# Optimization experiments

Hardware: AMD Instinct MI355X
Metric: run time of the kernel (lower is better)

Reference implementation:

```python
import jax, jax.numpy as jnp
import numpy as np

N_NODES = 50000
N_EDGES = 1600000
IN_CH, HID, OUT = 116, 256, 2


def setup_inputs() -> dict:
    key = jax.random.key(0)
    ks = jax.random.split(key, 8)
    x = jax.random.normal(ks[0], (N_NODES, IN_CH), dtype=jnp.float32)
    edge_index = jax.random.randint(ks[1], (2, N_EDGES), 0, N_NODES, dtype=jnp.int64)
    # GCNConv weights: layer l maps d_in -> d_out via x @ W + b (W stored [d_in, d_out])
    def glorot(k, di, do):
        s = jnp.sqrt(6.0 / (di + do)).astype(jnp.float32)
        return jax.random.uniform(k, (di, do), jnp.float32, -s, s)
    W1 = glorot(ks[2], IN_CH, HID); b1 = jnp.zeros((HID,), jnp.float32)
    W2 = glorot(ks[3], HID, HID);   b2 = jnp.zeros((HID,), jnp.float32)
    W3 = glorot(ks[4], HID, OUT);   b3 = jnp.zeros((OUT,), jnp.float32)
    return {"x": x, "edge_index": edge_index,
            "W1": W1, "b1": b1, "W2": W2, "b2": b2, "W3": W3, "b3": b3}


def _gcn_conv(h, W, b, src, dst, dinv):
    # PyG GCNConv (normalize=True, add_self_loops=True):
    #   out = D^{-1/2} (A + I) D^{-1/2} (h W) + b, deg counts in-edges + self loop
    hw = h @ W  # [N, d_out]
    coeff = dinv[src] * dinv[dst]                      # [E]
    msg = hw[src] * coeff[:, None]                     # [E, d_out]
    agg = jax.ops.segment_sum(msg, dst, num_segments=h.shape[0])
    agg = agg + hw * (dinv * dinv)[:, None]            # self-loop term
    return agg + b


def reference(x, edge_index, W1, b1, W2, b2, W3, b3):
    src, dst = edge_index[0], edge_index[1]
    n = x.shape[0]
    deg = jax.ops.segment_sum(jnp.ones_like(dst, dtype=x.dtype), dst, num_segments=n) + 1.0
    dinv = jax.lax.rsqrt(deg)
    h = jax.nn.relu(_gcn_conv(x, W1, b1, src, dst, dinv))
    h = jax.nn.relu(_gcn_conv(h, W2, b2, src, dst, dinv))
    out = _gcn_conv(h, W3, b3, src, dst, dinv)  # last layer: no activation (eval mode, no dropout)
    return out
```

## Files before the change

kernel.cpp:

```cpp
#include <hip/hip_runtime.h>
#include <hip/hip_bf16.h>
#include <stdint.h>

#define NN 50000
#define NE 1600000
#define INC 116
#define XBP 128
#define K1P 128
#define HID 256
#define OUTC 2

typedef float f32x4 __attribute__((ext_vector_type(4)));
typedef short s16x8 __attribute__((ext_vector_type(8)));

__device__ __forceinline__ ushort f2bf(float v) {
    uint32_t u = __float_as_uint(v);
    return (ushort)((u + 0x7FFFu + ((u >> 16) & 1u)) >> 16);
}
__device__ __forceinline__ float bf2f(ushort b) {
    return __uint_as_float(((uint32_t)b) << 16);
}
__device__ __forceinline__ float bflo(uint32_t u) { return __uint_as_float(u << 16); }
__device__ __forceinline__ float bfhi(uint32_t u) { return __uint_as_float(u & 0xFFFF0000u); }

__global__ void detect_fmt(const int* __restrict__ ebuf, int* __restrict__ flag) {
    int v = ebuf[2 * threadIdx.x + 1];
    unsigned long long b = __ballot(v != 0);
    if (threadIdx.x == 0) flag[0] = (b == 0ULL) ? 1 : 0;
}

__device__ __forceinline__ int edge_at(const int* __restrict__ ebuf, int is64, int idx) {
    return is64 ? ebuf[2 * idx] : ebuf[idx];
}

__global__ void deg_hist(const int* __restrict__ ebuf, const int* __restrict__ flag,
                         int* __restrict__ cnt) {
    int e = blockIdx.x * blockDim.x + threadIdx.x;
    if (e >= NE) return;
    int is64 = flag[0];
    int d = edge_at(ebuf, is64, NE + e);
    atomicAdd(&cnt[d], 1);
}

__global__ void dinv_kernel(const int* __restrict__ cnt, float* __restrict__ dinv) {
    int n = blockIdx.x * blockDim.x + threadIdx.x;
    if (n < NN) dinv[n] = rsqrtf((float)cnt[n] + 1.0f);
}

__global__ void scan1(const int* __restrict__ cnt, int* __restrict__ rowptr,
                      int* __restrict__ bsum) {
    __shared__ int s[256];
    int tid = threadIdx.x;
    int i = blockIdx.x * 256 + tid;
    int v = (i < NN) ? cnt[i] : 0;
    s[tid] = v;
    __syncthreads();
    for (int off = 1; off < 256; off <<= 1) {
        int t = (tid >= off) ? s[tid - off] : 0;
        __syncthreads();
        s[tid] += t;
        __syncthreads();
    }
    if (i < NN) rowptr[i] = s[tid] - v;
    if (tid == 255) bsum[blockIdx.x] = s[255];
}

__global__ void scan2(int* __restrict__ bsum, int nblocks) {
    __shared__ int s[256];
    int tid = threadIdx.x;
    int v = (tid < nblocks) ? bsum[tid] : 0;
    s[tid] = v;
    __syncthreads();
    for (int off = 1; off < 256; off <<= 1) {
        int t = (tid >= off) ? s[tid - off] : 0;
        __syncthreads();
        s[tid] += t;
        __syncthreads();
    }
    if (tid < nblocks) bsum[tid] = s[tid] - v;
}

__global__ void scan3(int* __restrict__ rowptr, const int* __restrict__ bsum,
                      int* __restrict__ fillpos) {
    int i = blockIdx.x * 256 + threadIdx.x;
    if (i < NN) {
        int r = rowptr[i] + bsum[blockIdx.x];
        rowptr[i] = r;
        fillpos[i] = r;
        if (i == NN - 1) rowptr[NN] = NE;
    }
}

__global__ void __launch_bounds__(256)
fill_csr2(const int* __restrict__ ebuf, const int* __restrict__ flag,
          int* __restrict__ fillpos, int* __restrict__ col) {
    int rng = blockIdx.x & 7;
    int lo = rng * (NN / 8), hi = lo + (NN / 8);
    int is64 = flag[0];
    int stride = (gridDim.x >> 3) * 256;
    for (int e = (blockIdx.x >> 3) * 256 + threadIdx.x; e < NE; e += stride) {
        int d = edge_at(ebuf, is64, NE + e);
        if (d >= lo && d < hi) {
            int s = edge_at(ebuf, is64, e);
            int p = atomicAdd(&fillpos[d], 1);
            col[p] = s;
        }
    }
}

__global__ void conv_x(const float* __restrict__ x, ushort* __restrict__ xb) {
    int i = blockIdx.x * 256 + threadIdx.x;
    if (i >= NN * XBP) return;
    int n = i >> 7, c = i & 127;
    xb[i] = (c < INC) ? f2bf(x[(size_t)n * INC + c]) : (ushort)0;
}

__global__ void decomp_w1(const float* __restrict__ W, ushort* __restrict__ hi,
                          ushort* __restrict__ lo) {
    int i = blockIdx.x * 256 + threadIdx.x;
    int n = i >> 7, k = i & 127;
    float v = (k < INC) ? W[k * HID + n] : 0.f;
    ushort h = f2bf(v);
    hi[n * K1P + k] = h;
    lo[n * K1P + k] = f2bf(v - bf2f(h));
}

__global__ void decomp_w2(const float* __restrict__ W, ushort* __restrict__ hi,
                          ushort* __restrict__ lo) {
    int i = blockIdx.x * 256 + threadIdx.x;
    int n = i >> 8, k = i & 255;
    float v = W[k * HID + n];
    ushort h = f2bf(v);
    hi[n * HID + k] = h;
    lo[n * HID + k] = f2bf(v - bf2f(h));
}

__global__ void __launch_bounds__(256)
agg1b(const ushort* __restrict__ xb, const float* __restrict__ x,
      const float* __restrict__ dinv, const int* __restrict__ rowptr,
      const int* __restrict__ col, ushort* __restrict__ ohi, ushort* __restrict__ olo) {
    __shared__ float red[16][16][8];
    int n = blockIdx.x, tid = threadIdx.x;
    int g = tid >> 4, c = tid & 15;
    int beg = rowptr[n], end = rowptr[n + 1];
    {
        float a0=0.f,a1=0.f,a2=0.f,a3=0.f,a4=0.f,a5=0.f,a6=0.f,a7=0.f;
        const ushort* hc = xb + c * 8;
        int j = beg + g;
        for (; j + 16 < end; j += 32) {
            int s0 = col[j], s1 = col[j + 16];
            float w0 = dinv[s0], w1 = dinv[s1];
            uint4 u0 = *(const uint4*)(hc + (size_t)s0 * XBP);
            uint4 u1 = *(const uint4*)(hc + (size_t)s1 * XBP);
            a0 += w0 * bflo(u0.x) + w1 * bflo(u1.x);
            a1 += w0 * bfhi(u0.x) + w1 * bfhi(u1.x);
            a2 += w0 * bflo(u0.y) + w1 * bflo(u1.y);
            a3 += w0 * bfhi(u0.y) + w1 * bfhi(u1.y);
            a4 += w0 * bflo(u0.z) + w1 * bflo(u1.z);
            a5 += w0 * bfhi(u0.z) + w1 * bfhi(u1.z);
            a6 += w0 * bflo(u0.w) + w1 * bflo(u1.w);
            a7 += w0 * bfhi(u0.w) + w1 * bfhi(u1.w);
        }
        if (j < end) {
            int s0 = col[j];
            float w0 = dinv[s0];
            uint4 u0 = *(const uint4*)(hc + (size_t)s0 * XBP);
            a0 += w0 * bflo(u0.x); a1 += w0 * bfhi(u0.x);
            a2 += w0 * bflo(u0.y); a3 += w0 * bfhi(u0.y);
            a4 += w0 * bflo(u0.z); a5 += w0 * bfhi(u0.z);
            a6 += w0 * bflo(u0.w); a7 += w0 * bfhi(u0.w);
        }
        red[g][c][0]=a0; red[g][c][1]=a1; red[g][c][2]=a2; red[g][c][3]=a3;
        red[g][c][4]=a4; red[g][c][5]=a5; red[g][c][6]=a6; red[g][c][7]=a7;
    }
    __syncthreads();
    int t = tid;
    if (t < K1P) {
        float s = 0.f;
        #pragma unroll
        for (int gg = 0; gg < 16; ++gg) s += red[gg][t >> 3][t & 7];
        float self = (t < INC) ? x[(size_t)n * INC + t] : 0.f;
        float dn = dinv[n];
        float r = dn * (s + dn * self);
        ushort h = f2bf(r);
        ohi[(size_t)n * K1P + t] = h;
        olo[(size_t)n * K1P + t] = f2bf(r - bf2f(h));
    }
}

__global__ void __launch_bounds__(256)
agg2b(const ushort* __restrict__ hb, const float* __restrict__ dinv,
      const int* __restrict__ rowptr, const int* __restrict__ col,
      ushort* __restrict__ ohi, ushort* __restrict__ olo) {
    __shared__ float red[8][32][8];
    int n = blockIdx.x, tid = threadIdx.x;
    int g = tid >> 5, c = tid & 31;
    int beg = rowptr[n], end = rowptr[n + 1];
    {
        float a0=0.f,a1=0.f,a2=0.f,a3=0.f,a4=0.f,a5=0.f,a6=0.f,a7=0.f;
        const ushort* hc = hb + c * 8;
        int j = beg + g;
        for (; j + 8 < end; j += 16) {
            int s0 = col[j], s1 = col[j + 8];
            float w0 = dinv[s0], w1 = dinv[s1];
            uint4 u0 = *(const uint4*)(hc + (size_t)s0 * HID);
            uint4 u1 = *(const uint4*)(hc + (size_t)s1 * HID);
            a0 += w0 * bflo(u0.x) + w1 * bflo(u1.x);
            a1 += w0 * bfhi(u0.x) + w1 * bfhi(u1.x);
            a2 += w0 * bflo(u0.y) + w1 * bflo(u1.y);
            a3 += w0 * bfhi(u0.y) + w1 * bfhi(u1.y);
            a4 += w0 * bflo(u0.z) + w1 * bflo(u1.z);
            a5 += w0 * bfhi(u0.z) + w1 * bfhi(u1.z);
            a6 += w0 * bflo(u0.w) + w1 * bflo(u1.w);
            a7 += w0 * bfhi(u0.w) + w1 * bfhi(u1.w);
        }
        if (j < end) {
            int s0 = col[j];
            float w0 = dinv[s0];
            uint4 u0 = *(const uint4*)(hc + (size_t)s0 * HID);
            a0 += w0 * bflo(u0.x); a1 += w0 * bfhi(u0.x);
            a2 += w0 * bflo(u0.y); a3 += w0 * bfhi(u0.y);
            a4 += w0 * bflo(u0.z); a5 += w0 * bfhi(u0.z);
            a6 += w0 * bflo(u0.w); a7 += w0 * bfhi(u0.w);
        }
        red[g][c][0]=a0; red[g][c][1]=a1; red[g][c][2]=a2; red[g][c][3]=a3;
        red[g][c][4]=a4; red[g][c][5]=a5; red[g][c][6]=a6; red[g][c][7]=a7;
    }
    __syncthreads();
    int t = tid;
    float s = 0.f;
    #pragma unroll
    for (int gg = 0; gg < 8; ++gg) s += red[gg][t >> 3][t & 7];
    float dn = dinv[n];
    float self = bf2f(hb[(size_t)n * HID + t]);
    float r = dn * (s + dn * self);
    ushort h = f2bf(r);
    ohi[(size_t)n * HID + t] = h;
    olo[(size_t)n * HID + t] = f2bf(r - bf2f(h));
}

template <int MODE>
__global__ void __launch_bounds__(256)
gemm_mfma(const ushort* __restrict__ Ahi, const ushort* __restrict__ Alo,
          const ushort* __restrict__ Bhi, const ushort* __restrict__ Blo,
          const float* __restrict__ bias, ushort* __restrict__ Cb,
          const float* __restrict__ W3, float* __restrict__ hw3,
          int M, int K, int Nn) {
    constexpr int BM = 128, BN = 128, BK = 32, LDK = BK + 8;
    __shared__ ushort sAh[BM * LDK], sAl[BM * LDK];
    __shared__ ushort sBh[BN * LDK], sBl[BN * LDK];
    int tid = threadIdx.x;
    int w = tid >> 6, l = tid & 63;
    int wr = w >> 1, wc = w & 1;
    int bm = blockIdx.x * BM, bn = blockIdx.y * BN;
    int l15 = l & 15, kg = l >> 4;
    f32x4 zero = {0.f, 0.f, 0.f, 0.f};
    f32x4 acc[4][4];
    #pragma unroll
    for (int i = 0; i < 4; ++i)
        #pragma unroll
        for (int j = 0; j < 4; ++j) acc[i][j] = zero;

    for (int kb = 0; kb < K; kb += BK) {
        #pragma unroll
        for (int it = 0; it < 2; ++it) {
            int cc = tid + it * 256;
            int row = cc >> 2, kp = (cc & 3) * 8;
            int ar = bm + row;
            float4 z4 = make_float4(0.f, 0.f, 0.f, 0.f);
            float4 avh = z4, avl = z4;
            if (ar < M) {
                avh = *(const float4*)(Ahi + (size_t)ar * K + kb + kp);
                avl = *(const float4*)(Alo + (size_t)ar * K + kb + kp);
            }
            *(float4*)&sAh[row * LDK + kp] = avh;
            *(float4*)&sAl[row * LDK + kp] = avl;
            int br = bn + row;
            float4 bvh = *(const float4*)(Bhi + (size_t)br * K + kb + kp);
            float4 bvl = *(const float4*)(Blo + (size_t)br * K + kb + kp);
            *(float4*)&sBh[row * LDK + kp] = bvh;
            *(float4*)&sBl[row * LDK + kp] = bvl;
        }
        __syncthreads();
        s16x8 ah[4], al[4], bh[4], bl[4];
        #pragma unroll
        for (int i = 0; i < 4; ++i) {
            int arow = wr * 64 + i * 16 + l15;
            ah[i] = *(const s16x8*)&sAh[arow * LDK + kg * 8];
            al[i] = *(const s16x8*)&sAl[arow * LDK + kg * 8];
            int brow = wc * 64 + i * 16 + l15;
            bh[i] = *(const s16x8*)&sBh[brow * LDK + kg * 8];
            bl[i] = *(const s16x8*)&sBl[brow * LDK + kg * 8];
        }
        #pragma unroll
        for (int i = 0; i < 4; ++i)
            #pragma unroll
            for (int j = 0; j < 4; ++j) {
                acc[i][j] = __builtin_amdgcn_mfma_f32_16x16x32_bf16(ah[i], bh[j], acc[i][j], 0, 0, 0);
                acc[i][j] = __builtin_amdgcn_mfma_f32_16x16x32_bf16(ah[i], bl[j], acc[i][j], 0, 0, 0);
                acc[i][j] = __builtin_amdgcn_mfma_f32_16x16x32_bf16(al[i], bh[j], acc[i][j], 0, 0, 0);
            }
        __syncthreads();
    }
    if (MODE == 1) {
        #pragma unroll
        for (int j = 0; j < 4; ++j) {
            int cn = bn + wc * 64 + j * 16 + l15;
            float bv = bias[cn];
            #pragma unroll
            for (int i = 0; i < 4; ++i) {
                int rbase = bm + wr * 64 + i * 16 + kg * 4;
                #pragma unroll
                for (int r = 0; r < 4; ++r) {
                    int rm = rbase + r;
                    if (rm < M) {
                        float v = fmaxf(acc[i][j][r] + bv, 0.f);
                        Cb[(size_t)rm * Nn + cn] = f2bf(v);
                    }
                }
            }
        }
    } else {
        float p0[4][4], p1[4][4];
        #pragma unroll
        for (int i = 0; i < 4; ++i)
            #pragma unroll
            for (int r = 0; r < 4; ++r) { p0[i][r] = 0.f; p1[i][r] = 0.f; }
        #pragma unroll
        for (int j = 0; j < 4; ++j) {
            int cn = bn + wc * 64 + j * 16 + l15;
            float bv = bias[cn];
            float w30 = W3[cn * 2 + 0], w31 = W3[cn * 2 + 1];
            #pragma unroll
            for (int i = 0; i < 4; ++i)
                #pragma unroll
                for (int r = 0; r < 4; ++r) {
                    float v = fmaxf(acc[i][j][r] + bv, 0.f);
                    p0[i][r] += v * w30;
                    p1[i][r] += v * w31;
                }
        }
        #pragma unroll
        for (int i = 0; i < 4; ++i)
            #pragma unroll
            for (int r = 0; r < 4; ++r) {
                float q0 = p0[i][r], q1 = p1[i][r];
                #pragma unroll
                for (int off = 1; off < 16; off <<= 1) {
                    q0 += __shfl_xor(q0, off);
                    q1 += __shfl_xor(q1, off);
                }
                if (l15 == 0) {
                    int rm = bm + wr * 64 + i * 16 + kg * 4 + r;
                    if (rm < M) {
                        atomicAdd(&hw3[rm * 2 + 0], q0);
                        atomicAdd(&hw3[rm * 2 + 1], q1);
                    }
                }
            }
    }
}

__global__ void agg3(const float* __restrict__ hw3, const float* __restrict__ dinv,
                     const int* __restrict__ rowptr, const int* __restrict__ col,
                     const float* __restrict__ b3, float* __restrict__ out) {
    int n = blockIdx.x * blockDim.x + threadIdx.x;
    if (n >= NN) return;
    float a0 = 0.f, a1 = 0.f;
    int beg = rowptr[n], end = rowptr[n + 1];
    for (int j = beg; j < end; ++j) {
        int s = col[j];
        float w = dinv[s];
        float2 v = ((const float2*)hw3)[s];
        a0 += w * v.x;
        a1 += w * v.y;
    }
    float dn = dinv[n];
    float2 sv = ((const float2*)hw3)[n];
    out[n * 2 + 0] = dn * (a0 + dn * sv.x) + b3[0];
    out[n * 2 + 1] = dn * (a1 + dn * sv.y) + b3[1];
}

extern "C" void kernel_launch(void* const* d_in, const int* in_sizes, int n_in,
                              void* d_out, int out_size, void* d_ws, size_t ws_size,
                              hipStream_t stream) {
    const float* x   = (const float*)d_in[0];
    const int*   ebf = (const int*)d_in[1];
    const float* W1  = (const float*)d_in[2];
    const float* b1  = (const float*)d_in[3];
    const float* W2  = (const float*)d_in[4];
    const float* b2  = (const float*)d_in[5];
    const float* W3  = (const float*)d_in[6];
    const float* b3  = (const float*)d_in[7];
    float* out = (float*)d_out;

    char* ws = (char*)d_ws;
    size_t off = 0;
    auto carve = [&](size_t bytes) -> char* {
        char* p = ws + off;
        off += (bytes + 255) & ~(size_t)255;
        return p;
    };
    int*    flag   = (int*)   carve(256);
    int*    cnt    = (int*)   carve((size_t)NN * 4);
    float*  dinv   = (float*) carve((size_t)NN * 4);
    int*    rowptr = (int*)   carve((size_t)(NN + 1) * 4);
    int*    fillpos= (int*)   carve((size_t)NN * 4);
    int*    bsum   = (int*)   carve(256 * 4);
    int*    col    = (int*)   carve((size_t)NE * 4);
    ushort* xb     = (ushort*)carve((size_t)NN * XBP * 2);
    ushort* W1thi  = (ushort*)carve((size_t)HID * K1P * 2);
    ushort* W1tlo  = (ushort*)carve((size_t)HID * K1P * 2);
    ushort* W2thi  = (ushort*)carve((size_t)HID * HID * 2);
    ushort* W2tlo  = (ushort*)carve((size_t)HID * HID * 2);
    ushort* a1hi   = (ushort*)carve((size_t)NN * K1P * 2);
    ushort* a1lo   = (ushort*)carve((size_t)NN * K1P * 2);
    ushort* h1b    = (ushort*)carve((size_t)NN * HID * 2);
    ushort* a2hi   = (ushort*)carve((size_t)NN * HID * 2);
    ushort* a2lo   = (ushort*)carve((size_t)NN * HID * 2);
    float*  hw3    = (float*) carve((size_t)NN * OUTC * 4);
    (void)ws_size; (void)n_in; (void)in_sizes; (void)out_size;

    const int SCAN_G = (NN + 255) / 256;
    const int EG     = (NE + 255) / 256;

    hipMemsetAsync(cnt, 0, (size_t)NN * 4, stream);
    hipMemsetAsync(hw3, 0, (size_t)NN * OUTC * 4, stream);
    detect_fmt<<<1, 64, 0, stream>>>(ebf, flag);
    deg_hist<<<EG, 256, 0, stream>>>(ebf, flag, cnt);
    dinv_kernel<<<SCAN_G, 256, 0, stream>>>(cnt, dinv);
    scan1<<<SCAN_G, 256, 0, stream>>>(cnt, rowptr, bsum);
    scan2<<<1, 256, 0, stream>>>(bsum, SCAN_G);
    scan3<<<SCAN_G, 256, 0, stream>>>(rowptr, bsum, fillpos);
    fill_csr2<<<2048, 256, 0, stream>>>(ebf, flag, fillpos, col);
    conv_x<<<((size_t)NN * XBP + 255) / 256, 256, 0, stream>>>(x, xb);
    decomp_w1<<<(HID * K1P) / 256, 256, 0, stream>>>(W1, W1thi, W1tlo);
    decomp_w2<<<(HID * HID) / 256, 256, 0, stream>>>(W2, W2thi, W2tlo);

    agg1b<<<NN, 256, 0, stream>>>(xb, x, dinv, rowptr, col, a1hi, a1lo);
    {
        dim3 g((NN + 127) / 128, HID / 128);
        gemm_mfma<1><<<g, 256, 0, stream>>>(a1hi, a1lo, W1thi, W1tlo, b1, h1b,
                                            nullptr, nullptr, NN, K1P, HID);
    }
    agg2b<<<NN, 256, 0, stream>>>(h1b, dinv, rowptr, col, a2hi, a2lo);
    {
        dim3 g((NN + 127) / 128, HID / 128);
        gemm_mfma<2><<<g, 256, 0, stream>>>(a2hi, a2lo, W2thi, W2tlo, b2, nullptr,
                                            W3, hw3, NN, HID, HID);
    }
    agg3<<<SCAN_G, 256, 0, stream>>>(hw3, dinv, rowptr, col, b3, out);
}
```

Measured before the change: 529.4 us.

## Store gather features in column panels and aggregate panel-by-panel for cache locality

The bf16 node features for layers 1 and 2 are now stored in column-panel layout (8 panels of 16 or 32 channels), written by conv_x and by the first GEMM epilogue. The aggregation kernels are restructured so each block processes one panel for a group of nodes, with a few threads per node, and the per-block shared-memory reduction is removed. Each panel is much smaller than the full feature matrix, so the random neighbor gathers should hit in L2 more often. The degree histogram also gets the same range-partitioned atomic scheme as fill_csr2. In exchange, col and rowptr are re-read once per panel, the GEMM epilogue stores are strided, and high-degree nodes now serialize across one or two threads.

```diff
diff --git a/kernel.cpp b/kernel.cpp
--- a/kernel.cpp
+++ b/kernel.cpp
@@ -5,7 +5,6 @@
 #define NN 50000
 #define NE 1600000
 #define INC 116
-#define XBP 128
 #define K1P 128
 #define HID 256
 #define OUTC 2
@@ -33,13 +32,17 @@
     return is64 ? ebuf[2 * idx] : ebuf[idx];
 }
 
-__global__ void deg_hist(const int* __restrict__ ebuf, const int* __restrict__ flag,
-                         int* __restrict__ cnt) {
-    int e = blockIdx.x * blockDim.x + threadIdx.x;
-    if (e >= NE) return;
+__global__ void __launch_bounds__(256)
+deg_hist2(const int* __restrict__ ebuf, const int* __restrict__ flag,
+          int* __restrict__ cnt) {
+    int rng = blockIdx.x & 7;
+    int lo = rng * (NN / 8), hi = lo + (NN / 8);
     int is64 = flag[0];
-    int d = edge_at(ebuf, is64, NE + e);
-    atomicAdd(&cnt[d], 1);
+    int stride = (gridDim.x >> 3) * 256;
+    for (int e = (blockIdx.x >> 3) * 256 + threadIdx.x; e < NE; e += stride) {
+        int d = edge_at(ebuf, is64, NE + e);
+        if (d >= lo && d < hi) atomicAdd(&cnt[d], 1);
+    }
 }
 
 __global__ void dinv_kernel(const int* __restrict__ cnt, float* __restrict__ dinv) {
@@ -108,11 +111,12 @@
     }
 }
 
-__global__ void conv_x(const float* __restrict__ x, ushort* __restrict__ xb) {
+__global__ void conv_x(const float* __restrict__ x, ushort* __restrict__ xp) {
     int i = blockIdx.x * 256 + threadIdx.x;
-    if (i >= NN * XBP) return;
+    if (i >= NN * K1P) return;
     int n = i >> 7, c = i & 127;
-    xb[i] = (c < INC) ? f2bf(x[(size_t)n * INC + c]) : (ushort)0;
+    ushort v = (c < INC) ? f2bf(x[(size_t)n * INC + c]) : (ushort)0;
+    xp[((size_t)(c >> 4) * NN + n) * 16 + (c & 15)] = v;
 }
 
 __global__ void decomp_w1(const float* __restrict__ W, ushort* __restrict__ hi,
@@ -136,107 +140,112 @@
 }
 
 __global__ void __launch_bounds__(256)
-agg1b(const ushort* __restrict__ xb, const float* __restrict__ x,
+agg1p(const ushort* __restrict__ xp, const float* __restrict__ x,
       const float* __restrict__ dinv, const int* __restrict__ rowptr,
       const int* __restrict__ col, ushort* __restrict__ ohi, ushort* __restrict__ olo) {
-    __shared__ float red[16][16][8];
-    int n = blockIdx.x, tid = threadIdx.x;
-    int g = tid >> 4, c = tid & 15;
+    int p = blockIdx.x & 7;
+    int nb = blockIdx.x >> 3;
+    int tid = threadIdx.x;
+    int g = tid >> 1, q = tid & 1;
+    int n = nb * 128 + g;
+    if (n >= NN) return;
+    const ushort* panel = xp + (size_t)p * NN * 16 + q * 8;
     int beg = rowptr[n], end = rowptr[n + 1];
-    {
-        float a0=0.f,a1=0.f,a2=0.f,a3=0.f,a4=0.f,a5=0.f,a6=0.f,a7=0.f;
-        const ushort* hc = xb + c * 8;
-        int j = beg + g;
-        for (; j + 16 < end; j += 32) {
-            int s0 = col[j], s1 = col[j + 16];
-            float w0 = dinv[s0], w1 = dinv[s1];
-            uint4 u0 = *(const uint4*)(hc + (size_t)s0 * XBP);
-            uint4 u1 = *(const uint4*)(hc + (size_t)s1 * XBP);
-            a0 += w0 * bflo(u0.x) + w1 * bflo(u1.x);
-            a1 += w0 * bfhi(u0.x) + w1 * bfhi(u1.x);
-            a2 += w0 * bflo(u0.y) + w1 * bflo(u1.y);
-            a3 += w0 * bfhi(u0.y) + w1 * bfhi(u1.y);
-            a4 += w0 * bflo(u0.z) + w1 * bflo(u1.z);
-            a5 += w0 * bfhi(u0.z) + w1 * bfhi(u1.z);
-            a6 += w0 * bflo(u0.w) + w1 * bflo(u1.w);
-            a7 += w0 * bfhi(u0.w) + w1 * bfhi(u1.w);
-        }
-        if (j < end) {
-            int s0 = col[j];
-            float w0 = dinv[s0];
-            uint4 u0 = *(const uint4*)(hc + (size_t)s0 * XBP);
-            a0 += w0 * bflo(u0.x); a1 += w0 * bfhi(u0.x);
-            a2 += w0 * bflo(u0.y); a3 += w0 * bfhi(u0.y);
-            a4 += w0 * bflo(u0.z); a5 += w0 * bfhi(u0.z);
-            a6 += w0 * bflo(u0.w); a7 += w0 * bfhi(u0.w);
-        }
-        red[g][c][0]=a0; red[g][c][1]=a1; red[g][c][2]=a2; red[g][c][3]=a3;
-        red[g][c][4]=a4; red[g][c][5]=a5; red[g][c][6]=a6; red[g][c][7]=a7;
-    }
-    __syncthreads();
-    int t = tid;
-    if (t < K1P) {
-        float s = 0.f;
-        #pragma unroll
-        for (int gg = 0; gg < 16; ++gg) s += red[gg][t >> 3][t & 7];
-        float self = (t < INC) ? x[(size_t)n * INC + t] : 0.f;
-        float dn = dinv[n];
-        float r = dn * (s + dn * self);
+    float a0=0.f,a1=0.f,a2=0.f,a3=0.f,a4=0.f,a5=0.f,a6=0.f,a7=0.f;
+    int j = beg;
+    for (; j + 1 < end; j += 2) {
+        int s0 = col[j], s1 = col[j + 1];
+        float w0 = dinv[s0], w1 = dinv[s1];
+        uint4 u0 = *(const uint4*)(panel + (size_t)s0 * 16);
+        uint4 u1 = *(const uint4*)(panel + (size_t)s1 * 16);
+        a0 += w0 * bflo(u0.x) + w1 * bflo(u1.x);
+        a1 += w0 * bfhi(u0.x) + w1 * bfhi(u1.x);
+        a2 += w0 * bflo(u0.y) + w1 * bflo(u1.y);
+        a3 += w0 * bfhi(u0.y) + w1 * bfhi(u1.y);
+        a4 += w0 * bflo(u0.z) + w1 * bflo(u1.z);
+        a5 += w0 * bfhi(u0.z) + w1 * bfhi(u1.z);
+        a6 += w0 * bflo(u0.w) + w1 * bflo(u1.w);
+        a7 += w0 * bfhi(u0.w) + w1 * bfhi(u1.w);
+    }
+    if (j < end) {
+        int s0 = col[j];
+        float w0 = dinv[s0];
+        uint4 u0 = *(const uint4*)(panel + (size_t)s0 * 16);
+        a0 += w0 * bflo(u0.x); a1 += w0 * bfhi(u0.x);
+        a2 += w0 * bflo(u0.y); a3 += w0 * bfhi(u0.y);
+        a4 += w0 * bflo(u0.z); a5 += w0 * bfhi(u0.z);
+        a6 += w0 * bflo(u0.w); a7 += w0 * bfhi(u0.w);
+    }
+    int cbase = p * 16 + q * 8;
+    float dn = dinv[n];
+    float acc[8] = {a0,a1,a2,a3,a4,a5,a6,a7};
+    ushort hs[8], ls[8];
+    #pragma unroll
+    for (int i = 0; i < 8; ++i) {
+        int ch = cbase + i;
+        float self = (ch < INC) ? x[(size_t)n * INC + ch] : 0.f;
+        float r = dn * (acc[i] + dn * self);
         ushort h = f2bf(r);
-        ohi[(size_t)n * K1P + t] = h;
-        olo[(size_t)n * K1P + t] = f2bf(r - bf2f(h));
-    }
+        hs[i] = h;
+        ls[i] = f2bf(r - bf2f(h));
+    }
+    *(uint4*)(ohi + (size_t)n * K1P + cbase) = *(uint4*)hs;
+    *(uint4*)(olo + (size_t)n * K1P + cbase) = *(uint4*)ls;
 }
 
 __global__ void __launch_bounds__(256)
-agg2b(const ushort* __restrict__ hb, const float* __restrict__ dinv,
+agg2p(const ushort* __restrict__ h1p, const float* __restrict__ dinv,
       const int* __restrict__ rowptr, const int* __restrict__ col,
       ushort* __restrict__ ohi, ushort* __restrict__ olo) {
-    __shared__ float red[8][32][8];
-    int n = blockIdx.x, tid = threadIdx.x;
-    int g = tid >> 5, c = tid & 31;
+    int p = blockIdx.x & 7;
+    int nb = blockIdx.x >> 3;
+    int tid = threadIdx.x;
+    int g = tid >> 2, q = tid & 3;
+    int n = nb * 64 + g;
+    if (n >= NN) return;
+    const ushort* panel = h1p + (size_t)p * NN * 32 + q * 8;
     int beg = rowptr[n], end = rowptr[n + 1];
-    {
-        float a0=0.f,a1=0.f,a2=0.f,a3=0.f,a4=0.f,a5=0.f,a6=0.f,a7=0.f;
-        const ushort* hc = hb + c * 8;
-        int j = beg + g;
-        for (; j + 8 < end; j += 16) {
-            int s0 = col[j], s1 = col[j + 8];
-            float w0 = dinv[s0], w1 = dinv[s1];
-            uint4 u0 = *(const uint4*)(hc + (size_t)s0 * HID);
-            uint4 u1 = *(const uint4*)(hc + (size_t)s1 * HID);
-            a0 += w0 * bflo(u0.x) + w1 * bflo(u1.x);
-            a1 += w0 * bfhi(u0.x) + w1 * bfhi(u1.x);
-            a2 += w0 * bflo(u0.y) + w1 * bflo(u1.y);
-            a3 += w0 * bfhi(u0.y) + w1 * bfhi(u1.y);
-            a4 += w0 * bflo(u0.z) + w1 * bflo(u1.z);
-            a5 += w0 * bfhi(u0.z) + w1 * bfhi(u1.z);
-            a6 += w0 * bflo(u0.w) + w1 * bflo(u1.w);
-            a7 += w0 * bfhi(u0.w) + w1 * bfhi(u1.w);
-        }
-        if (j < end) {
-            int s0 = col[j];
-            float w0 = dinv[s0];
-            uint4 u0 = *(const uint4*)(hc + (size_t)s0 * HID);
-            a0 += w0 * bflo(u0.x); a1 += w0 * bfhi(u0.x);
-            a2 += w0 * bflo(u0.y); a3 += w0 * bfhi(u0.y);
-            a4 += w0 * bflo(u0.z); a5 += w0 * bfhi(u0.z);
-            a6 += w0 * bflo(u0.w); a7 += w0 * bfhi(u0.w);
-        }
-        red[g][c][0]=a0; red[g][c][1]=a1; red[g][c][2]=a2; red[g][c][3]=a3;
-        red[g][c][4]=a4; red[g][c][5]=a5; red[g][c][6]=a6; red[g][c][7]=a7;
-    }
-    __syncthreads();
-    int t = tid;
-    float s = 0.f;
+    float a0=0.f,a1=0.f,a2=0.f,a3=0.f,a4=0.f,a5=0.f,a6=0.f,a7=0.f;
+    int j = beg;
+    for (; j + 1 < end; j += 2) {
+        int s0 = col[j], s1 = col[j + 1];
+        float w0 = dinv[s0], w1 = dinv[s1];
+        uint4 u0 = *(const uint4*)(panel + (size_t)s0 * 32);
+        uint4 u1 = *(const uint4*)(panel + (size_t)s1 * 32);
+        a0 += w0 * bflo(u0.x) + w1 * bflo(u1.x);
+        a1 += w0 * bfhi(u0.x) + w1 * bfhi(u1.x);
+        a2 += w0 * bflo(u0.y) + w1 * bflo(u1.y);
+        a3 += w0 * bfhi(u0.y) + w1 * bfhi(u1.y);
+        a4 += w0 * bflo(u0.z) + w1 * bflo(u1.z);
+        a5 += w0 * bfhi(u0.z) + w1 * bfhi(u1.z);
+        a6 += w0 * bflo(u0.w) + w1 * bflo(u1.w);
+        a7 += w0 * bfhi(u0.w) + w1 * bfhi(u1.w);
+    }
+    if (j < end) {
+        int s0 = col[j];
+        float w0 = dinv[s0];
+        uint4 u0 = *(const uint4*)(panel + (size_t)s0 * 32);
+        a0 += w0 * bflo(u0.x); a1 += w0 * bfhi(u0.x);
+        a2 += w0 * bflo(u0.y); a3 += w0 * bfhi(u0.y);
+        a4 += w0 * bflo(u0.z); a5 += w0 * bfhi(u0.z);
+        a6 += w0 * bflo(u0.w); a7 += w0 * bfhi(u0.w);
+    }
+    float dn = dinv[n];
+    uint4 us = *(const uint4*)(panel + (size_t)n * 32);
+    float self[8] = {bflo(us.x),bfhi(us.x),bflo(us.y),bfhi(us.y),
+                     bflo(us.z),bfhi(us.z),bflo(us.w),bfhi(us.w)};
+    float acc[8] = {a0,a1,a2,a3,a4,a5,a6,a7};
+    ushort hs[8], ls[8];
     #pragma unroll
-    for (int gg = 0; gg < 8; ++gg) s += red[gg][t >> 3][t & 7];
-    float dn = dinv[n];
-    float self = bf2f(hb[(size_t)n * HID + t]);
-    float r = dn * (s + dn * self);
-    ushort h = f2bf(r);
-    ohi[(size_t)n * HID + t] = h;
-    olo[(size_t)n * HID + t] = f2bf(r - bf2f(h));
+    for (int i = 0; i < 8; ++i) {
+        float r = dn * (acc[i] + dn * self[i]);
+        ushort h = f2bf(r);
+        hs[i] = h;
+        ls[i] = f2bf(r - bf2f(h));
+    }
+    int cbase = p * 32 + q * 8;
+    *(uint4*)(ohi + (size_t)n * HID + cbase) = *(uint4*)hs;
+    *(uint4*)(olo + (size_t)n * HID + cbase) = *(uint4*)ls;
 }
 
 template <int MODE>
@@ -307,6 +316,7 @@
         for (int j = 0; j < 4; ++j) {
             int cn = bn + wc * 64 + j * 16 + l15;
             float bv = bias[cn];
+            size_t pbase = ((size_t)(cn >> 5) * NN) * 32 + (cn & 31);
             #pragma unroll
             for (int i = 0; i < 4; ++i) {
                 int rbase = bm + wr * 64 + i * 16 + kg * 4;
@@ -315,7 +325,7 @@
                     int rm = rbase + r;
                     if (rm < M) {
                         float v = fmaxf(acc[i][j][r] + bv, 0.f);
-                        Cb[(size_t)rm * Nn + cn] = f2bf(v);
+                        Cb[pbase + (size_t)rm * 32] = f2bf(v);
                     }
                 }
             }
@@ -408,42 +418,41 @@
     int*    fillpos= (int*)   carve((size_t)NN * 4);
     int*    bsum   = (int*)   carve(256 * 4);
     int*    col    = (int*)   carve((size_t)NE * 4);
-    ushort* xb     = (ushort*)carve((size_t)NN * XBP * 2);
+    ushort* xp     = (ushort*)carve((size_t)NN * K1P * 2);
     ushort* W1thi  = (ushort*)carve((size_t)HID * K1P * 2);
     ushort* W1tlo  = (ushort*)carve((size_t)HID * K1P * 2);
     ushort* W2thi  = (ushort*)carve((size_t)HID * HID * 2);
     ushort* W2tlo  = (ushort*)carve((size_t)HID * HID * 2);
     ushort* a1hi   = (ushort*)carve((size_t)NN * K1P * 2);
     ushort* a1lo   = (ushort*)carve((size_t)NN * K1P * 2);
-    ushort* h1b    = (ushort*)carve((size_t)NN * HID * 2);
+    ushort* h1p    = (ushort*)carve((size_t)NN * HID * 2);
     ushort* a2hi   = (ushort*)carve((size_t)NN * HID * 2);
     ushort* a2lo   = (ushort*)carve((size_t)NN * HID * 2);
     float*  hw3    = (float*) carve((size_t)NN * OUTC * 4);
     (void)ws_size; (void)n_in; (void)in_sizes; (void)out_size;
 
     const int SCAN_G = (NN + 255) / 256;
-    const int EG     = (NE + 255) / 256;
 
     hipMemsetAsync(cnt, 0, (size_t)NN * 4, stream);
     hipMemsetAsync(hw3, 0, (size_t)NN * OUTC * 4, stream);
     detect_fmt<<<1, 64, 0, stream>>>(ebf, flag);
-    deg_hist<<<EG, 256, 0, stream>>>(ebf, flag, cnt);
+    deg_hist2<<<2048, 256, 0, stream>>>(ebf, flag, cnt);
     dinv_kernel<<<SCAN_G, 256, 0, stream>>>(cnt, dinv);
     scan1<<<SCAN_G, 256, 0, stream>>>(cnt, rowptr, bsum);
     scan2<<<1, 256, 0, stream>>>(bsum, SCAN_G);
     scan3<<<SCAN_G, 256, 0, stream>>>(rowptr, bsum, fillpos);
     fill_csr2<<<2048, 256, 0, stream>>>(ebf, flag, fillpos, col);
-    conv_x<<<((size_t)NN * XBP + 255) / 256, 256, 0, stream>>>(x, xb);
+    conv_x<<<((size_t)NN * K1P + 255) / 256, 256, 0, stream>>>(x, xp);
     decomp_w1<<<(HID * K1P) / 256, 256, 0, stream>>>(W1, W1thi, W1tlo);
     decomp_w2<<<(HID * HID) / 256, 256, 0, stream>>>(W2, W2thi, W2tlo);
 
-    agg1b<<<NN, 256, 0, stream>>>(xb, x, dinv, rowptr, col, a1hi, a1lo);
+    agg1p<<<8 * ((NN + 127) / 128), 256, 0, stream>>>(xp, x, dinv, rowptr, col, a1hi, a1lo);
     {
         dim3 g((NN + 127) / 128, HID / 128);
-        gemm_mfma<1><<<g, 256, 0, stream>>>(a1hi, a1lo, W1thi, W1tlo, b1, h1b,
+        gemm_mfma<1><<<g, 256, 0, stream>>>(a1hi, a1lo, W1thi, W1tlo, b1, h1p,
                                             nullptr, nullptr, NN, K1P, HID);
     }
-    agg2b<<<NN, 256, 0, stream>>>(h1b, dinv, rowptr, col, a2hi, a2lo);
+    agg2p<<<8 * ((NN + 63) / 64), 256, 0, stream>>>(h1p, dinv, rowptr, col, a2hi, a2lo);
     {
         dim3 g((NN + 127) / 128, HID / 128);
         gemm_mfma<2><<<g, 256, 0, stream>>>(a2hi, a2lo, W2thi, W2tlo, b2, nullptr,
```

Measured after the change: 691.4 us. 30.6% more time.

## Bucket CSR edges by source tile and sync aggregation across tiles for cache locality

Applied to the files above, without the earlier changes.

Each destination row's edges are split into 13 buckets by source node range (4096 nodes each), using a per-(node,tile) histogram, prefix and fill. The aggregation kernels now give each thread group several nodes and walk the source tiles in lockstep, with a block barrier after each tile. The goal is to keep the gathered feature rows of one source tile resident in cache across the block. In exchange there are extra setup passes, a 13x larger count array, more serial per-node work with no intra-node parallel reduction, and load imbalance between nodes.

```diff
diff --git a/kernel.cpp b/kernel.cpp
--- a/kernel.cpp
+++ b/kernel.cpp
@@ -9,6 +9,8 @@
 #define K1P 128
 #define HID 256
 #define OUTC 2
+#define NT 13
+#define TSH 12
 
 typedef float f32x4 __attribute__((ext_vector_type(4)));
 typedef short s16x8 __attribute__((ext_vector_type(8)));
@@ -33,18 +35,31 @@
     return is64 ? ebuf[2 * idx] : ebuf[idx];
 }
 
-__global__ void deg_hist(const int* __restrict__ ebuf, const int* __restrict__ flag,
-                         int* __restrict__ cnt) {
-    int e = blockIdx.x * blockDim.x + threadIdx.x;
-    if (e >= NE) return;
+__global__ void __launch_bounds__(256)
+deg_hist3(const int* __restrict__ ebuf, const int* __restrict__ flag,
+          int* __restrict__ cnt2) {
+    int rng = blockIdx.x & 7;
+    int lo = rng * (NN / 8), hi = lo + (NN / 8);
     int is64 = flag[0];
-    int d = edge_at(ebuf, is64, NE + e);
-    atomicAdd(&cnt[d], 1);
-}
-
-__global__ void dinv_kernel(const int* __restrict__ cnt, float* __restrict__ dinv) {
-    int n = blockIdx.x * blockDim.x + threadIdx.x;
-    if (n < NN) dinv[n] = rsqrtf((float)cnt[n] + 1.0f);
+    int stride = (gridDim.x >> 3) * 256;
+    for (int e = (blockIdx.x >> 3) * 256 + threadIdx.x; e < NE; e += stride) {
+        int d = edge_at(ebuf, is64, NE + e);
+        if (d >= lo && d < hi) {
+            int s = edge_at(ebuf, is64, e);
+            atomicAdd(&cnt2[d * NT + (s >> TSH)], 1);
+        }
+    }
+}
+
+__global__ void sum_cnt(const int* __restrict__ cnt2, int* __restrict__ cnt,
+                        float* __restrict__ dinv) {
+    int n = blockIdx.x * 256 + threadIdx.x;
+    if (n >= NN) return;
+    int s = 0;
+    #pragma unroll
+    for (int t = 0; t < NT; ++t) s += cnt2[n * NT + t];
+    cnt[n] = s;
+    dinv[n] = rsqrtf((float)s + 1.0f);
 }
 
 __global__ void scan1(const int* __restrict__ cnt, int* __restrict__ rowptr,
@@ -80,20 +95,31 @@
     if (tid < nblocks) bsum[tid] = s[tid] - v;
 }
 
-__global__ void scan3(int* __restrict__ rowptr, const int* __restrict__ bsum,
-                      int* __restrict__ fillpos) {
+__global__ void scan3(int* __restrict__ rowptr, const int* __restrict__ bsum) {
     int i = blockIdx.x * 256 + threadIdx.x;
     if (i < NN) {
-        int r = rowptr[i] + bsum[blockIdx.x];
-        rowptr[i] = r;
-        fillpos[i] = r;
+        rowptr[i] += bsum[blockIdx.x];
         if (i == NN - 1) rowptr[NN] = NE;
     }
 }
 
+__global__ void mk_rowptr2(const int* __restrict__ rowptr, const int* __restrict__ cnt2,
+                           int* __restrict__ rp2, int* __restrict__ fillpos2) {
+    int n = blockIdx.x * 256 + threadIdx.x;
+    if (n >= NN) return;
+    int running = rowptr[n];
+    #pragma unroll
+    for (int t = 0; t < NT; ++t) {
+        rp2[n * NT + t] = running;
+        fillpos2[n * NT + t] = running;
+        running += cnt2[n * NT + t];
+    }
+    if (n == NN - 1) rp2[NN * NT] = NE;
+}
+
 __global__ void __launch_bounds__(256)
-fill_csr2(const int* __restrict__ ebuf, const int* __restrict__ flag,
-          int* __restrict__ fillpos, int* __restrict__ col) {
+fill_csr3(const int* __restrict__ ebuf, const int* __restrict__ flag,
+          int* __restrict__ fillpos2, int* __restrict__ col) {
     int rng = blockIdx.x & 7;
     int lo = rng * (NN / 8), hi = lo + (NN / 8);
     int is64 = flag[0];
@@ -102,7 +128,7 @@
         int d = edge_at(ebuf, is64, NE + e);
         if (d >= lo && d < hi) {
             int s = edge_at(ebuf, is64, e);
-            int p = atomicAdd(&fillpos[d], 1);
+            int p = atomicAdd(&fillpos2[d * NT + (s >> TSH)], 1);
             col[p] = s;
         }
     }
@@ -136,107 +162,138 @@
 }
 
 __global__ void __launch_bounds__(256)
-agg1b(const ushort* __restrict__ xb, const float* __restrict__ x,
-      const float* __restrict__ dinv, const int* __restrict__ rowptr,
+agg1t(const ushort* __restrict__ xb, const float* __restrict__ x,
+      const float* __restrict__ dinv, const int* __restrict__ rp2,
       const int* __restrict__ col, ushort* __restrict__ ohi, ushort* __restrict__ olo) {
-    __shared__ float red[16][16][8];
-    int n = blockIdx.x, tid = threadIdx.x;
+    int tid = threadIdx.x;
     int g = tid >> 4, c = tid & 15;
-    int beg = rowptr[n], end = rowptr[n + 1];
-    {
-        float a0=0.f,a1=0.f,a2=0.f,a3=0.f,a4=0.f,a5=0.f,a6=0.f,a7=0.f;
-        const ushort* hc = xb + c * 8;
-        int j = beg + g;
-        for (; j + 16 < end; j += 32) {
-            int s0 = col[j], s1 = col[j + 16];
-            float w0 = dinv[s0], w1 = dinv[s1];
-            uint4 u0 = *(const uint4*)(hc + (size_t)s0 * XBP);
-            uint4 u1 = *(const uint4*)(hc + (size_t)s1 * XBP);
-            a0 += w0 * bflo(u0.x) + w1 * bflo(u1.x);
-            a1 += w0 * bfhi(u0.x) + w1 * bfhi(u1.x);
-            a2 += w0 * bflo(u0.y) + w1 * bflo(u1.y);
-            a3 += w0 * bfhi(u0.y) + w1 * bfhi(u1.y);
-            a4 += w0 * bflo(u0.z) + w1 * bflo(u1.z);
-            a5 += w0 * bfhi(u0.z) + w1 * bfhi(u1.z);
-            a6 += w0 * bflo(u0.w) + w1 * bflo(u1.w);
-            a7 += w0 * bfhi(u0.w) + w1 * bfhi(u1.w);
-        }
-        if (j < end) {
-            int s0 = col[j];
-            float w0 = dinv[s0];
-            uint4 u0 = *(const uint4*)(hc + (size_t)s0 * XBP);
-            a0 += w0 * bflo(u0.x); a1 += w0 * bfhi(u0.x);
-            a2 += w0 * bflo(u0.y); a3 += w0 * bfhi(u0.y);
-            a4 += w0 * bflo(u0.z); a5 += w0 * bfhi(u0.z);
-            a6 += w0 * bflo(u0.w); a7 += w0 * bfhi(u0.w);
-        }
-        red[g][c][0]=a0; red[g][c][1]=a1; red[g][c][2]=a2; red[g][c][3]=a3;
-        red[g][c][4]=a4; red[g][c][5]=a5; red[g][c][6]=a6; red[g][c][7]=a7;
-    }
-    __syncthreads();
-    int t = tid;
-    if (t < K1P) {
-        float s = 0.f;
-        #pragma unroll
-        for (int gg = 0; gg < 16; ++gg) s += red[gg][t >> 3][t & 7];
-        float self = (t < INC) ? x[(size_t)n * INC + t] : 0.f;
+    int nbase = blockIdx.x * 32 + g * 2;
+    const ushort* hc = xb + c * 8;
+    float acc[2][8];
+    #pragma unroll
+    for (int i = 0; i < 2; ++i)
+        #pragma unroll
+        for (int k = 0; k < 8; ++k) acc[i][k] = 0.f;
+    for (int t = 0; t < NT; ++t) {
+        #pragma unroll
+        for (int i = 0; i < 2; ++i) {
+            int n = nbase + i;
+            if (n < NN) {
+                int beg = rp2[n * NT + t], end = rp2[n * NT + t + 1];
+                int j = beg;
+                for (; j + 1 < end; j += 2) {
+                    int s0 = col[j], s1 = col[j + 1];
+                    float w0 = dinv[s0], w1 = dinv[s1];
+                    uint4 u0 = *(const uint4*)(hc + (size_t)s0 * XBP);
+                    uint4 u1 = *(const uint4*)(hc + (size_t)s1 * XBP);
+                    acc[i][0] += w0 * bflo(u0.x) + w1 * bflo(u1.x);
+                    acc[i][1] += w0 * bfhi(u0.x) + w1 * bfhi(u1.x);
+                    acc[i][2] += w0 * bflo(u0.y) + w1 * bflo(u1.y);
+                    acc[i][3] += w0 * bfhi(u0.y) + w1 * bfhi(u1.y);
+                    acc[i][4] += w0 * bflo(u0.z) + w1 * bflo(u1.z);
+                    acc[i][5] += w0 * bfhi(u0.z) + w1 * bfhi(u1.z);
+                    acc[i][6] += w0 * bflo(u0.w) + w1 * bflo(u1.w);
+                    acc[i][7] += w0 * bfhi(u0.w) + w1 * bfhi(u1.w);
+                }
+                if (j < end) {
+                    int s0 = col[j];
+                    float w0 = dinv[s0];
+                    uint4 u0 = *(const uint4*)(hc + (size_t)s0 * XBP);
+                    acc[i][0] += w0 * bflo(u0.x); acc[i][1] += w0 * bfhi(u0.x);
+                    acc[i][2] += w0 * bflo(u0.y); acc[i][3] += w0 * bfhi(u0.y);
+                    acc[i][4] += w0 * bflo(u0.z); acc[i][5] += w0 * bfhi(u0.z);
+                    acc[i][6] += w0 * bflo(u0.w); acc[i][7] += w0 * bfhi(u0.w);
+                }
+            }
+        }
+        __syncthreads();
+    }
+    #pragma unroll
+    for (int i = 0; i < 2; ++i) {
+        int n = nbase + i;
+        if (n >= NN) continue;
         float dn = dinv[n];
-        float r = dn * (s + dn * self);
-        ushort h = f2bf(r);
-        ohi[(size_t)n * K1P + t] = h;
-        olo[(size_t)n * K1P + t] = f2bf(r - bf2f(h));
+        ushort hs[8], ls[8];
+        #pragma unroll
+        for (int k = 0; k < 8; ++k) {
+            int ch = c * 8 + k;
+            float self = (ch < INC) ? x[(size_t)n * INC + ch] : 0.f;
+            float r = dn * (acc[i][k] + dn * self);
+            ushort h = f2bf(r);
+            hs[k] = h;
+            ls[k] = f2bf(r - bf2f(h));
+        }
+        *(uint4*)(ohi + (size_t)n * K1P + c * 8) = *(uint4*)hs;
+        *(uint4*)(olo + (size_t)n * K1P + c * 8) = *(uint4*)ls;
     }
 }
 
 __global__ void __launch_bounds__(256)
-agg2b(const ushort* __restrict__ hb, const float* __restrict__ dinv,
-      const int* __restrict__ rowptr, const int* __restrict__ col,
+agg2t(const ushort* __restrict__ hb, const float* __restrict__ dinv,
+      const int* __restrict__ rp2, const int* __restrict__ col,
       ushort* __restrict__ ohi, ushort* __restrict__ olo) {
-    __shared__ float red[8][32][8];
-    int n = blockIdx.x, tid = threadIdx.x;
+    int tid = threadIdx.x;
     int g = tid >> 5, c = tid & 31;
-    int beg = rowptr[n], end = rowptr[n + 1];
-    {
-        float a0=0.f,a1=0.f,a2=0.f,a3=0.f,a4=0.f,a5=0.f,a6=0.f,a7=0.f;
-        const ushort* hc = hb + c * 8;
-        int j = beg + g;
-        for (; j + 8 < end; j += 16) {
-            int s0 = col[j], s1 = col[j + 8];
-            float w0 = dinv[s0], w1 = dinv[s1];
-            uint4 u0 = *(const uint4*)(hc + (size_t)s0 * HID);
-            uint4 u1 = *(const uint4*)(hc + (size_t)s1 * HID);
-            a0 += w0 * bflo(u0.x) + w1 * bflo(u1.x);
-            a1 += w0 * bfhi(u0.x) + w1 * bfhi(u1.x);
-            a2 += w0 * bflo(u0.y) + w1 * bflo(u1.y);
-            a3 += w0 * bfhi(u0.y) + w1 * bfhi(u1.y);
-            a4 += w0 * bflo(u0.z) + w1 * bflo(u1.z);
-            a5 += w0 * bfhi(u0.z) + w1 * bfhi(u1.z);
-            a6 += w0 * bflo(u0.w) + w1 * bflo(u1.w);
-            a7 += w0 * bfhi(u0.w) + w1 * bfhi(u1.w);
-        }
-        if (j < end) {
-            int s0 = col[j];
-            float w0 = dinv[s0];
-            uint4 u0 = *(const uint4*)(hc + (size_t)s0 * HID);
-            a0 += w0 * bflo(u0.x); a1 += w0 * bfhi(u0.x);
-            a2 += w0 * bflo(u0.y); a3 += w0 * bfhi(u0.y);
-            a4 += w0 * bflo(u0.z); a5 += w0 * bfhi(u0.z);
-            a6 += w0 * bflo(u0.w); a7 += w0 * bfhi(u0.w);
-        }
-        red[g][c][0]=a0; red[g][c][1]=a1; red[g][c][2]=a2; red[g][c][3]=a3;
-        red[g][c][4]=a4; red[g][c][5]=a5; red[g][c][6]=a6; red[g][c][7]=a7;
-    }
-    __syncthreads();
-    int t = tid;
-    float s = 0.f;
-    #pragma unroll
-    for (int gg = 0; gg < 8; ++gg) s += red[gg][t >> 3][t & 7];
-    float dn = dinv[n];
-    float self = bf2f(hb[(size_t)n * HID + t]);
-    float r = dn * (s + dn * self);
-    ushort h = f2bf(r);
-    ohi[(size_t)n * HID + t] = h;
-    olo[(size_t)n * HID + t] = f2bf(r - bf2f(h));
+    int nbase = blockIdx.x * 32 + g * 4;
+    const ushort* hc = hb + c * 8;
+    float acc[4][8];
+    #pragma unroll
+    for (int i = 0; i < 4; ++i)
+        #pragma unroll
+        for (int k = 0; k < 8; ++k) acc[i][k] = 0.f;
+    for (int t = 0; t < NT; ++t) {
+        #pragma unroll
+        for (int i = 0; i < 4; ++i) {
+            int n = nbase + i;
+            if (n < NN) {
+                int beg = rp2[n * NT + t], end = rp2[n * NT + t + 1];
+                int j = beg;
+                for (; j + 1 < end; j += 2) {
+                    int s0 = col[j], s1 = col[j + 1];
+                    float w0 = dinv[s0], w1 = dinv[s1];
+                    uint4 u0 = *(const uint4*)(hc + (size_t)s0 * HID);
+                    uint4 u1 = *(const uint4*)(hc + (size_t)s1 * HID);
+                    acc[i][0] += w0 * bflo(u0.x) + w1 * bflo(u1.x);
+                    acc[i][1] += w0 * bfhi(u0.x) + w1 * bfhi(u1.x);
+                    acc[i][2] += w0 * bflo(u0.y) + w1 * bflo(u1.y);
+                    acc[i][3] += w0 * bfhi(u0.y) + w1 * bfhi(u1.y);
+                    acc[i][4] += w0 * bflo(u0.z) + w1 * bflo(u1.z);
+                    acc[i][5] += w0 * bfhi(u0.z) + w1 * bfhi(u1.z);
+                    acc[i][6] += w0 * bflo(u0.w) + w1 * bflo(u1.w);
+                    acc[i][7] += w0 * bfhi(u0.w) + w1 * bfhi(u1.w);
+                }
+                if (j < end) {
+                    int s0 = col[j];
+                    float w0 = dinv[s0];
+                    uint4 u0 = *(const uint4*)(hc + (size_t)s0 * HID);
+                    acc[i][0] += w0 * bflo(u0.x); acc[i][1] += w0 * bfhi(u0.x);
+                    acc[i][2] += w0 * bflo(u0.y); acc[i][3] += w0 * bfhi(u0.y);
+                    acc[i][4] += w0 * bflo(u0.z); acc[i][5] += w0 * bfhi(u0.z);
+                    acc[i][6] += w0 * bflo(u0.w); acc[i][7] += w0 * bfhi(u0.w);
+                }
+            }
+        }
+        __syncthreads();
+    }
+    #pragma unroll
+    for (int i = 0; i < 4; ++i) {
+        int n = nbase + i;
+        if (n >= NN) continue;
+        float dn = dinv[n];
+        uint4 us = *(const uint4*)(hc + (size_t)n * HID);
+        float self[8] = {bflo(us.x),bfhi(us.x),bflo(us.y),bfhi(us.y),
+                         bflo(us.z),bfhi(us.z),bflo(us.w),bfhi(us.w)};
+        ushort hs[8], ls[8];
+        #pragma unroll
+        for (int k = 0; k < 8; ++k) {
+            float r = dn * (acc[i][k] + dn * self[k]);
+            ushort h = f2bf(r);
+            hs[k] = h;
+            ls[k] = f2bf(r - bf2f(h));
+        }
+        *(uint4*)(ohi + (size_t)n * HID + c * 8) = *(uint4*)hs;
+        *(uint4*)(olo + (size_t)n * HID + c * 8) = *(uint4*)ls;
+    }
 }
 
 template <int MODE>
@@ -401,49 +458,52 @@
         off += (bytes + 255) & ~(size_t)255;
         return p;
     };
-    int*    flag   = (int*)   carve(256);
-    int*    cnt    = (int*)   carve((size_t)NN * 4);
-    float*  dinv   = (float*) carve((size_t)NN * 4);
-    int*    rowptr = (int*)   carve((size_t)(NN + 1) * 4);
-    int*    fillpos= (int*)   carve((size_t)NN * 4);
-    int*    bsum   = (int*)   carve(256 * 4);
-    int*    col    = (int*)   carve((size_t)NE * 4);
-    ushort* xb     = (ushort*)carve((size_t)NN * XBP * 2);
-    ushort* W1thi  = (ushort*)carve((size_t)HID * K1P * 2);
-    ushort* W1tlo  = (ushort*)carve((size_t)HID * K1P * 2);
-    ushort* W2thi  = (ushort*)carve((size_t)HID * HID * 2);
-    ushort* W2tlo  = (ushort*)carve((size_t)HID * HID * 2);
-    ushort* a1hi   = (ushort*)carve((size_t)NN * K1P * 2);
-    ushort* a1lo   = (ushort*)carve((size_t)NN * K1P * 2);
-    ushort* h1b    = (ushort*)carve((size_t)NN * HID * 2);
-    ushort* a2hi   = (ushort*)carve((size_t)NN * HID * 2);
-    ushort* a2lo   = (ushort*)carve((size_t)NN * HID * 2);
-    float*  hw3    = (float*) carve((size_t)NN * OUTC * 4);
+    int*    flag    = (int*)   carve(256);
+    int*    cnt     = (int*)   carve((size_t)NN * 4);
+    int*    cnt2    = (int*)   carve((size_t)NN * NT * 4);
+    float*  dinv    = (float*) carve((size_t)NN * 4);
+    int*    rowptr  = (int*)   carve((size_t)(NN + 1) * 4);
+    int*    rp2     = (int*)   carve((size_t)(NN * NT + 1) * 4);
+    int*    fillpos2= (int*)   carve((size_t)NN * NT * 4);
+    int*    bsum    = (int*)   carve(256 * 4);
+    int*    col     = (int*)   carve((size_t)NE * 4);
+    ushort* xb      = (ushort*)carve((size_t)NN * XBP * 2);
+    ushort* W1thi   = (ushort*)carve((size_t)HID * K1P * 2);
+    ushort* W1tlo   = (ushort*)carve((size_t)HID * K1P * 2);
+    ushort* W2thi   = (ushort*)carve((size_t)HID * HID * 2);
+    ushort* W2tlo   = (ushort*)carve((size_t)HID * HID * 2);
+    ushort* a1hi    = (ushort*)carve((size_t)NN * K1P * 2);
+    ushort* a1lo    = (ushort*)carve((size_t)NN * K1P * 2);
+    ushort* h1b     = (ushort*)carve((size_t)NN * HID * 2);
+    ushort* a2hi    = (ushort*)carve((size_t)NN * HID * 2);
+    ushort* a2lo    = (ushort*)carve((size_t)NN * HID * 2);
+    float*  hw3     = (float*) carve((size_t)NN * OUTC * 4);
     (void)ws_size; (void)n_in; (void)in_sizes; (void)out_size;
 
     const int SCAN_G = (NN + 255) / 256;
-    const int EG     = (NE + 255) / 256;
-
-    hipMemsetAsync(cnt, 0, (size_t)NN * 4, stream);
+    const int AGG_G  = (NN + 31) / 32;
+
+    hipMemsetAsync(cnt2, 0, (size_t)NN * NT * 4, stream);
     hipMemsetAsync(hw3, 0, (size_t)NN * OUTC * 4, stream);
     detect_fmt<<<1, 64, 0, stream>>>(ebf, flag);
-    deg_hist<<<EG, 256, 0, stream>>>(ebf, flag, cnt);
-    dinv_kernel<<<SCAN_G, 256, 0, stream>>>(cnt, dinv);
+    deg_hist3<<<2048, 256, 0, stream>>>(ebf, flag, cnt2);
+    sum_cnt<<<SCAN_G, 256, 0, stream>>>(cnt2, cnt, dinv);
     scan1<<<SCAN_G, 256, 0, stream>>>(cnt, rowptr, bsum);
     scan2<<<1, 256, 0, stream>>>(bsum, SCAN_G);
-    scan3<<<SCAN_G, 256, 0, stream>>>(rowptr, bsum, fillpos);
-    fill_csr2<<<2048, 256, 0, stream>>>(ebf, flag, fillpos, col);
+    scan3<<<SCAN_G, 256, 0, stream>>>(rowptr, bsum);
+    mk_rowptr2<<<SCAN_G, 256, 0, stream>>>(rowptr, cnt2, rp2, fillpos2);
+    fill_csr3<<<2048, 256, 0, stream>>>(ebf, flag, fillpos2, col);
     conv_x<<<((size_t)NN * XBP + 255) / 256, 256, 0, stream>>>(x, xb);
     decomp_w1<<<(HID * K1P) / 256, 256, 0, stream>>>(W1, W1thi, W1tlo);
     decomp_w2<<<(HID * HID) / 256, 256, 0, stream>>>(W2, W2thi, W2tlo);
 
-    agg1b<<<NN, 256, 0, stream>>>(xb, x, dinv, rowptr, col, a1hi, a1lo);
+    agg1t<<<AGG_G, 256, 0, stream>>>(xb, x, dinv, rp2, col, a1hi, a1lo);
     {
         dim3 g((NN + 127) / 128, HID / 128);
         gemm_mfma<1><<<g, 256, 0, stream>>>(a1hi, a1lo, W1thi, W1tlo, b1, h1b,
                                             nullptr, nullptr, NN, K1P, HID);
     }
-    agg2b<<<NN, 256, 0, stream>>>(h1b, dinv, rowptr, col, a2hi, a2lo);
+    agg2t<<<AGG_G, 256, 0, stream>>>(h1b, dinv, rp2, col, a2hi, a2lo);
     {
         dim3 g((NN + 127) / 128, HID / 128);
         gemm_mfma<2><<<g, 256, 0, stream>>>(a2hi, a2lo, W2thi, W2tlo, b2, nullptr,
```

Measured after the change: 569.6 us. 1.08x slower.
